# Performance work log

Measured on AMD Instinct MI355X. Metric: run time of the kernel, lower is better.

## Reference

```python
import jax, jax.numpy as jnp
import numpy as np

X_SIZE = 256
H_SIZE = 512
N_CHILDREN = 32768


def setup_inputs() -> dict:
    key = jax.random.key(0)
    ks = jax.random.split(key, 7)
    x = jax.random.normal(ks[0], (X_SIZE,), dtype=jnp.float32)
    hs = jax.random.normal(ks[1], (N_CHILDREN, H_SIZE), dtype=jnp.float32)
    cs = jax.random.normal(ks[2], (N_CHILDREN, H_SIZE), dtype=jnp.float32)
    # xavier-uniform-ish init for weights, zeros for biases
    def xavier(k, shape):
        fan_in, fan_out = shape[-1], shape[-2]
        limit = float(np.sqrt(6.0 / (fan_in + fan_out)))
        return jax.random.uniform(k, shape, jnp.float32, -limit, limit)
    w_iou = xavier(ks[3], (3, H_SIZE, X_SIZE))
    u_iou = xavier(ks[4], (3, H_SIZE, H_SIZE))
    b_iou = jnp.zeros((3, H_SIZE), jnp.float32)
    w_f = xavier(ks[5], (H_SIZE, X_SIZE))
    u_f = xavier(ks[6], (H_SIZE, H_SIZE))
    b_f = jnp.zeros((H_SIZE, 1), jnp.float32)
    return {"x": x, "hs": hs, "cs": cs, "w_iou": w_iou, "u_iou": u_iou,
            "b_iou": b_iou, "w_f": w_f, "u_f": u_f, "b_f": b_f}


def reference(x, hs, cs, w_iou, u_iou, b_iou, w_f, u_f, b_f):
    # Child-sum Tree-LSTM cell for a single node.
    h_sum = hs.sum(axis=0)                                    # (h,)
    iou = (jnp.einsum('khx,x->kh', w_iou, x)
           + jnp.einsum('khg,g->kh', u_iou, h_sum)
           + b_iou)                                            # (3, h)
    i, o, u = iou[0], iou[1], iou[2]
    # fs: (h, n_children) forget gates, one per child
    fs = (w_f @ x)[:, None] + jnp.einsum('hg,ng->hn', u_f, hs) + b_f
    i = jax.nn.sigmoid(i)
    o = jax.nn.sigmoid(o)
    fs = jax.nn.sigmoid(fs)
    u = jnp.tanh(u)
    c = i * u + jnp.sum(fs * cs.T, axis=1)                    # (h,)
    h = o * jnp.tanh(c)
    return (h, c)
```

## Files before the change

### kernel.cpp

```cpp
#include <hip/hip_runtime.h>
#include <stdint.h>
#include <stddef.h>

#define H 512
#define XD 256
#define NCHLD 32768
#define NB 64
#define NSHARD 32

#define WS_PREF 0
#define WS_IOU  512
#define WS_CACC 2048
#define WS_HSUM 18432
#define WS_UF16 34816

typedef float f32x4 __attribute__((ext_vector_type(4)));
typedef _Float16 f16x8 __attribute__((ext_vector_type(8)));
typedef _Float16 f16x4 __attribute__((ext_vector_type(4)));

__device__ __forceinline__ float sigm(float x) { return 1.0f / (1.0f + __expf(-x)); }

__global__ __launch_bounds__(256) void k0_setup(const float* __restrict__ x,
                                                const float* __restrict__ w_f,
                                                const float* __restrict__ b_f,
                                                const float* __restrict__ u_f,
                                                float* __restrict__ ws) {
    const int b = blockIdx.x;
    if (b < 256) {
        const int i = (b * 256 + threadIdx.x) * 4;
        float4 v = *(const float4*)(u_f + i);
        f16x4 h;
        h[0] = (_Float16)v.x; h[1] = (_Float16)v.y;
        h[2] = (_Float16)v.z; h[3] = (_Float16)v.w;
        *(f16x4*)((_Float16*)(ws + WS_UF16) + i) = h;
    } else {
        const int gid = (b - 256) * 256 + threadIdx.x;
        const int row = gid >> 2;
        const int part = gid & 3;
        const float4* wr = (const float4*)(w_f + (size_t)row * XD) + part * 16;
        const float4* xv = (const float4*)x + part * 16;
        float acc = 0.0f;
#pragma unroll 4
        for (int i = 0; i < 16; ++i) {
            float4 a = wr[i], c = xv[i];
            acc += a.x * c.x + a.y * c.y + a.z * c.z + a.w * c.w;
        }
        acc += __shfl_xor(acc, 1);
        acc += __shfl_xor(acc, 2);
        if (part == 0) ws[WS_PREF + row] = acc + b_f[row];
        float4 z = make_float4(0.f, 0.f, 0.f, 0.f);
#pragma unroll
        for (int t = 0; t < 4; ++t)
            ((float4*)ws)[512 + gid * 4 + t] = z;
    }
}

__global__ __launch_bounds__(256) void k1_hsum(const float* __restrict__ hs,
                                               float* __restrict__ ws) {
    __shared__ float red[2][H];
    const int t = threadIdx.x;
    const int b = blockIdx.x;
    const float4* src = (const float4*)hs + (size_t)b * 64 * 128 + (t >> 7) * 128 + (t & 127);
    float4 a = make_float4(0.f, 0.f, 0.f, 0.f);
#pragma unroll
    for (int i = 0; i < 32; ++i) {
        float4 v = src[(size_t)i * 256];
        a.x += v.x; a.y += v.y; a.z += v.z; a.w += v.w;
    }
    *(float4*)&red[t >> 7][(t & 127) * 4] = a;
    __syncthreads();
    float* shard = ws + WS_HSUM + (b & (NSHARD - 1)) * H;
    atomicAdd(&shard[t],       red[0][t]       + red[1][t]);
    atomicAdd(&shard[t + 256], red[0][t + 256] + red[1][t + 256]);
}

__global__ __launch_bounds__(512, 4) void k2_main(const float* __restrict__ hs,
                                                  const float* __restrict__ cs,
                                                  float* __restrict__ ws) {
    __shared__ _Float16 Bs[NB * H];

    const _Float16* uf16 = (const _Float16*)(ws + WS_UF16);
    const float* pre_f = ws + WS_PREF;
    float* c_acc = ws + WS_CACC + (blockIdx.x & (NSHARD - 1)) * H;

    const int tid  = threadIdx.x;
    const int wid  = tid >> 6;
    const int lane = tid & 63;
    const int c0   = blockIdx.x * NB;
    const int fc   = lane & 15;
    const int q    = lane >> 4;

    {
        const float4* g0 = (const float4*)hs + (((size_t)(c0 + wid)) << 7) + (lane << 1);
        _Float16* w0 = Bs + (wid << 9) + ((lane ^ wid) << 3);
        float4 r0[8], r1[8];
#pragma unroll
        for (int j = 0; j < 4; ++j) {
            r0[2 * j]     = g0[(size_t)j << 10];
            r0[2 * j + 1] = g0[((size_t)j << 10) + 1];
        }
#pragma unroll
        for (int j = 0; j < 4; ++j) {
            r1[2 * j]     = g0[(size_t)(j + 4) << 10];
            r1[2 * j + 1] = g0[((size_t)(j + 4) << 10) + 1];
        }
#pragma unroll
        for (int j = 0; j < 4; ++j) {
            f16x8 hv;
            hv[0] = (_Float16)r0[2*j].x;   hv[1] = (_Float16)r0[2*j].y;
            hv[2] = (_Float16)r0[2*j].z;   hv[3] = (_Float16)r0[2*j].w;
            hv[4] = (_Float16)r0[2*j+1].x; hv[5] = (_Float16)r0[2*j+1].y;
            hv[6] = (_Float16)r0[2*j+1].z; hv[7] = (_Float16)r0[2*j+1].w;
            *(f16x8*)(w0 + (j << 12)) = hv;
        }
#pragma unroll
        for (int j = 0; j < 4; ++j) {
            f16x8 hv;
            hv[0] = (_Float16)r1[2*j].x;   hv[1] = (_Float16)r1[2*j].y;
            hv[2] = (_Float16)r1[2*j].z;   hv[3] = (_Float16)r1[2*j].w;
            hv[4] = (_Float16)r1[2*j+1].x; hv[5] = (_Float16)r1[2*j+1].y;
            hv[6] = (_Float16)r1[2*j+1].z; hv[7] = (_Float16)r1[2*j+1].w;
            *(f16x8*)(w0 + ((j + 4) << 12)) = hv;
        }
    }
    __syncthreads();

    f32x4 acc[4][4];
    const f32x4 vzero = {0.0f, 0.0f, 0.0f, 0.0f};
#pragma unroll
    for (int rt = 0; rt < 4; ++rt)
#pragma unroll
        for (int ct = 0; ct < 4; ++ct)
            acc[rt][ct] = vzero;

    const _Float16* abase = uf16 + (size_t)(wid * 64 + fc) * H + q * 8;

#pragma unroll
    for (int kk = 0; kk < 16; ++kk) {
        f16x8 af[4];
#pragma unroll
        for (int rt = 0; rt < 4; ++rt)
            af[rt] = *(const f16x8*)(abase + (size_t)rt * 16 * H + kk * 32);
        f16x8 bf[4];
#pragma unroll
        for (int ct = 0; ct < 4; ++ct) {
            const int ch = ct * 16 + fc;
            bf[ct] = *(const f16x8*)(Bs + ch * H + (((kk * 4 + q) ^ (fc & 7)) << 3));
        }
#pragma unroll
        for (int ct = 0; ct < 4; ++ct)
#pragma unroll
            for (int rt = 0; rt < 4; ++rt)
                acc[rt][ct] = __builtin_amdgcn_mfma_f32_16x16x32_f16(af[rt], bf[ct], acc[rt][ct], 0, 0, 0);
    }

#pragma unroll
    for (int rt = 0; rt < 4; ++rt) {
        const int rglob = wid * 64 + rt * 16 + q * 4;
        float4 pf = *(const float4*)(pre_f + rglob);
        f32x4 csum = vzero;
#pragma unroll
        for (int ct = 0; ct < 4; ++ct) {
            const int child = c0 + ct * 16 + fc;
            float4 cv = *(const float4*)(cs + (size_t)child * H + rglob);
            csum[0] += sigm(acc[rt][ct][0] + pf.x) * cv.x;
            csum[1] += sigm(acc[rt][ct][1] + pf.y) * cv.y;
            csum[2] += sigm(acc[rt][ct][2] + pf.z) * cv.z;
            csum[3] += sigm(acc[rt][ct][3] + pf.w) * cv.w;
        }
#pragma unroll
        for (int m = 1; m <= 8; m <<= 1) {
            csum[0] += __shfl_xor(csum[0], m); csum[1] += __shfl_xor(csum[1], m);
            csum[2] += __shfl_xor(csum[2], m); csum[3] += __shfl_xor(csum[3], m);
        }
        if (fc == 0) {
            atomicAdd(&c_acc[rglob + 0], csum[0]); atomicAdd(&c_acc[rglob + 1], csum[1]);
            atomicAdd(&c_acc[rglob + 2], csum[2]); atomicAdd(&c_acc[rglob + 3], csum[3]);
        }
    }
}

__global__ __launch_bounds__(256) void k3_iou(const float* __restrict__ x,
                                              const float* __restrict__ w_iou,
                                              const float* __restrict__ u_iou,
                                              const float* __restrict__ b_iou,
                                              float* __restrict__ ws) {
    __shared__ float h_red[H];
    const int tid = threadIdx.x;
    {
        float a0 = 0.0f, a1 = 0.0f;
#pragma unroll 8
        for (int s = 0; s < NSHARD; ++s) {
            a0 += ws[WS_HSUM + s * H + tid * 2 + 0];
            a1 += ws[WS_HSUM + s * H + tid * 2 + 1];
        }
        h_red[tid * 2 + 0] = a0;
        h_red[tid * 2 + 1] = a1;
    }
    __syncthreads();

    const int gid = blockIdx.x * 256 + tid;
    const int row = gid >> 4;
    const int part = gid & 15;
    float acc = 0.0f;
    const float4* wr = (const float4*)(w_iou + (size_t)row * XD) + part * 4;
    const float4* xv = (const float4*)x + part * 4;
#pragma unroll
    for (int i = 0; i < 4; ++i) {
        float4 a = wr[i], b = xv[i];
        acc += a.x * b.x + a.y * b.y + a.z * b.z + a.w * b.w;
    }
    const float4* ur = (const float4*)(u_iou + (size_t)row * H) + part * 8;
    const float4* hv = (const float4*)h_red + part * 8;
#pragma unroll
    for (int i = 0; i < 8; ++i) {
        float4 a = ur[i], b = hv[i];
        acc += a.x * b.x + a.y * b.y + a.z * b.z + a.w * b.w;
    }
    acc += __shfl_xor(acc, 1);
    acc += __shfl_xor(acc, 2);
    acc += __shfl_xor(acc, 4);
    acc += __shfl_xor(acc, 8);
    if (part == 0) ws[WS_IOU + row] = acc + b_iou[row];
}

__global__ __launch_bounds__(512) void k4_fin(const float* __restrict__ ws,
                                              float* __restrict__ out) {
    const int h = threadIdx.x;
    float cacc = 0.0f;
#pragma unroll 8
    for (int s = 0; s < NSHARD; ++s) cacc += ws[WS_CACC + s * H + h];
    const float i = sigm(ws[WS_IOU + h]);
    const float o = sigm(ws[WS_IOU + 512 + h]);
    const float u = tanhf(ws[WS_IOU + 1024 + h]);
    const float c = i * u + cacc;
    out[h]       = o * tanhf(c);
    out[512 + h] = c;
}

extern "C" void kernel_launch(void* const* d_in, const int* in_sizes, int n_in,
                              void* d_out, int out_size, void* d_ws, size_t ws_size,
                              hipStream_t stream) {
    const float* x     = (const float*)d_in[0];
    const float* hs    = (const float*)d_in[1];
    const float* cs    = (const float*)d_in[2];
    const float* w_iou = (const float*)d_in[3];
    const float* u_iou = (const float*)d_in[4];
    const float* b_iou = (const float*)d_in[5];
    const float* w_f   = (const float*)d_in[6];
    const float* u_f   = (const float*)d_in[7];
    const float* b_f   = (const float*)d_in[8];
    float* ws  = (float*)d_ws;
    float* out = (float*)d_out;

    k0_setup<<<264, 256, 0, stream>>>(x, w_f, b_f, u_f, ws);
    k1_hsum<<<512, 256, 0, stream>>>(hs, ws);
    k2_main<<<NCHLD / NB, 512, 0, stream>>>(hs, cs, ws);
    k3_iou<<<96, 256, 0, stream>>>(x, w_iou, u_iou, b_iou, ws);
    k4_fin<<<1, 512, 0, stream>>>(ws, out);
}
```

Measured before the change: 220.9 us.

## Fuse child hidden-state sum into main kernel and prefetch cs before MFMA loop

Removes the separate hs-sum kernel and instead accumulates the column sums of hs while the main kernel already loads hs tiles to convert them to fp16. Each block reduces into shared memory and adds into sharded global accumulators. The cs tile is loaded into registers before the matrix loop so its latency overlaps with compute. Occupancy hint drops from 4 to 2 blocks per CU to make room for the extra 64 registers, at the cost of less latency hiding. The shared-memory atomics add some contention.

```diff
diff --git a/kernel.cpp b/kernel.cpp
--- a/kernel.cpp
+++ b/kernel.cpp
@@ -55,33 +55,16 @@
     }
 }
 
-__global__ __launch_bounds__(256) void k1_hsum(const float* __restrict__ hs,
-                                               float* __restrict__ ws) {
-    __shared__ float red[2][H];
-    const int t = threadIdx.x;
-    const int b = blockIdx.x;
-    const float4* src = (const float4*)hs + (size_t)b * 64 * 128 + (t >> 7) * 128 + (t & 127);
-    float4 a = make_float4(0.f, 0.f, 0.f, 0.f);
-#pragma unroll
-    for (int i = 0; i < 32; ++i) {
-        float4 v = src[(size_t)i * 256];
-        a.x += v.x; a.y += v.y; a.z += v.z; a.w += v.w;
-    }
-    *(float4*)&red[t >> 7][(t & 127) * 4] = a;
-    __syncthreads();
-    float* shard = ws + WS_HSUM + (b & (NSHARD - 1)) * H;
-    atomicAdd(&shard[t],       red[0][t]       + red[1][t]);
-    atomicAdd(&shard[t + 256], red[0][t + 256] + red[1][t + 256]);
-}
-
-__global__ __launch_bounds__(512, 4) void k2_main(const float* __restrict__ hs,
+__global__ __launch_bounds__(512, 2) void k2_main(const float* __restrict__ hs,
                                                   const float* __restrict__ cs,
                                                   float* __restrict__ ws) {
     __shared__ _Float16 Bs[NB * H];
+    __shared__ float hsum_l[H];
 
     const _Float16* uf16 = (const _Float16*)(ws + WS_UF16);
     const float* pre_f = ws + WS_PREF;
-    float* c_acc = ws + WS_CACC + (blockIdx.x & (NSHARD - 1)) * H;
+    float* c_acc   = ws + WS_CACC + (blockIdx.x & (NSHARD - 1)) * H;
+    float* h_shard = ws + WS_HSUM + (blockIdx.x & (NSHARD - 1)) * H;
 
     const int tid  = threadIdx.x;
     const int wid  = tid >> 6;
@@ -90,40 +73,51 @@
     const int fc   = lane & 15;
     const int q    = lane >> 4;
 
+    hsum_l[tid] = 0.0f;
+    __syncthreads();
+
     {
         const float4* g0 = (const float4*)hs + (((size_t)(c0 + wid)) << 7) + (lane << 1);
         _Float16* w0 = Bs + (wid << 9) + ((lane ^ wid) << 3);
-        float4 r0[8], r1[8];
-#pragma unroll
-        for (int j = 0; j < 4; ++j) {
-            r0[2 * j]     = g0[(size_t)j << 10];
-            r0[2 * j + 1] = g0[((size_t)j << 10) + 1];
-        }
-#pragma unroll
-        for (int j = 0; j < 4; ++j) {
-            r1[2 * j]     = g0[(size_t)(j + 4) << 10];
-            r1[2 * j + 1] = g0[((size_t)(j + 4) << 10) + 1];
-        }
-#pragma unroll
-        for (int j = 0; j < 4; ++j) {
+        float4 r[16];
+#pragma unroll
+        for (int j = 0; j < 8; ++j) {
+            r[2 * j]     = g0[(size_t)j << 10];
+            r[2 * j + 1] = g0[((size_t)j << 10) + 1];
+        }
+        float4 ha = make_float4(0.f, 0.f, 0.f, 0.f);
+        float4 hb = make_float4(0.f, 0.f, 0.f, 0.f);
+#pragma unroll
+        for (int j = 0; j < 8; ++j) {
+            float4 lo = r[2 * j], hi = r[2 * j + 1];
             f16x8 hv;
-            hv[0] = (_Float16)r0[2*j].x;   hv[1] = (_Float16)r0[2*j].y;
-            hv[2] = (_Float16)r0[2*j].z;   hv[3] = (_Float16)r0[2*j].w;
-            hv[4] = (_Float16)r0[2*j+1].x; hv[5] = (_Float16)r0[2*j+1].y;
-            hv[6] = (_Float16)r0[2*j+1].z; hv[7] = (_Float16)r0[2*j+1].w;
+            hv[0] = (_Float16)lo.x; hv[1] = (_Float16)lo.y;
+            hv[2] = (_Float16)lo.z; hv[3] = (_Float16)lo.w;
+            hv[4] = (_Float16)hi.x; hv[5] = (_Float16)hi.y;
+            hv[6] = (_Float16)hi.z; hv[7] = (_Float16)hi.w;
             *(f16x8*)(w0 + (j << 12)) = hv;
-        }
-#pragma unroll
-        for (int j = 0; j < 4; ++j) {
-            f16x8 hv;
-            hv[0] = (_Float16)r1[2*j].x;   hv[1] = (_Float16)r1[2*j].y;
-            hv[2] = (_Float16)r1[2*j].z;   hv[3] = (_Float16)r1[2*j].w;
-            hv[4] = (_Float16)r1[2*j+1].x; hv[5] = (_Float16)r1[2*j+1].y;
-            hv[6] = (_Float16)r1[2*j+1].z; hv[7] = (_Float16)r1[2*j+1].w;
-            *(f16x8*)(w0 + ((j + 4) << 12)) = hv;
-        }
+            ha.x += lo.x; ha.y += lo.y; ha.z += lo.z; ha.w += lo.w;
+            hb.x += hi.x; hb.y += hi.y; hb.z += hi.z; hb.w += hi.w;
+        }
+        float* hd = &hsum_l[lane * 8];
+        atomicAdd(hd + 0, ha.x); atomicAdd(hd + 1, ha.y);
+        atomicAdd(hd + 2, ha.z); atomicAdd(hd + 3, ha.w);
+        atomicAdd(hd + 4, hb.x); atomicAdd(hd + 5, hb.y);
+        atomicAdd(hd + 6, hb.z); atomicAdd(hd + 7, hb.w);
     }
     __syncthreads();
+
+    atomicAdd(&h_shard[tid], hsum_l[tid]);
+
+    float4 csr[4][4];
+#pragma unroll
+    for (int rt = 0; rt < 4; ++rt)
+#pragma unroll
+        for (int ct = 0; ct < 4; ++ct) {
+            const int child = c0 + ct * 16 + fc;
+            const int rglob = wid * 64 + rt * 16 + q * 4;
+            csr[rt][ct] = *(const float4*)(cs + (size_t)child * H + rglob);
+        }
 
     f32x4 acc[4][4];
     const f32x4 vzero = {0.0f, 0.0f, 0.0f, 0.0f};
@@ -161,8 +155,7 @@
         f32x4 csum = vzero;
 #pragma unroll
         for (int ct = 0; ct < 4; ++ct) {
-            const int child = c0 + ct * 16 + fc;
-            float4 cv = *(const float4*)(cs + (size_t)child * H + rglob);
+            float4 cv = csr[rt][ct];
             csum[0] += sigm(acc[rt][ct][0] + pf.x) * cv.x;
             csum[1] += sigm(acc[rt][ct][1] + pf.y) * cv.y;
             csum[2] += sigm(acc[rt][ct][2] + pf.z) * cv.z;
@@ -254,7 +247,6 @@
     float* out = (float*)d_out;
 
     k0_setup<<<264, 256, 0, stream>>>(x, w_f, b_f, u_f, ws);
-    k1_hsum<<<512, 256, 0, stream>>>(hs, ws);
     k2_main<<<NCHLD / NB, 512, 0, stream>>>(hs, cs, ws);
     k3_iou<<<96, 256, 0, stream>>>(x, w_iou, u_iou, b_iou, ws);
     k4_fin<<<1, 512, 0, stream>>>(ws, out);
```

After: 215.4 us. 1.03x faster.
